# Optimization experiments

Hardware: AMD Instinct MI355X
Metric: run time of the kernel (lower is better)

The kernel has to match this reference:

```python
import jax, jax.numpy as jnp
import numpy as np

D = 512; N = 4096; NH = 16; DEPTH = 3; MLP = 4; GENES = 250; GH = 64; GW = 64


def setup_inputs() -> dict:
    key = jax.random.key(0)
    ks = jax.random.split(key, 10)
    gf = jax.random.normal(ks[0], (N, D), jnp.float32)
    # unique spot positions: permutation of the 64x64 grid cells
    perm = jax.random.permutation(ks[1], GH * GW)[:N]
    coords = jnp.stack([perm // GW, perm % GW], axis=1).astype(jnp.int32)
    s = 0.02
    rn = lambda k, sh: jax.random.normal(k, sh, jnp.float32) * s
    return dict(
        global_feats=gf, coords=coords, grid_h=GH, grid_w=GW,
        ln1_g=jnp.ones((DEPTH, D)), ln1_b=jnp.zeros((DEPTH, D)),
        wqkv=rn(ks[2], (DEPTH, 3 * D, D)), bqkv=jnp.zeros((DEPTH, 3 * D)),
        wo=rn(ks[3], (DEPTH, D, D)), bo=jnp.zeros((DEPTH, D)),
        ln2_g=jnp.ones((DEPTH, D)), ln2_b=jnp.zeros((DEPTH, D)),
        w1=rn(ks[4], (DEPTH, MLP * D, D)), b1=jnp.zeros((DEPTH, MLP * D)),
        w2=rn(ks[5], (DEPTH, D, MLP * D)), b2=jnp.zeros((DEPTH, D)),
        ck=rn(ks[6], (DEPTH, D, 1, 3, 3)), cb=jnp.zeros((DEPTH, D)),
        lnf_g=jnp.ones((D,)), lnf_b=jnp.zeros((D,)),
        wp=rn(ks[7], (GENES, D)), bp=jnp.zeros((GENES,)),
    )


def _ln(x, g, b, eps=1e-5):
    m = jnp.mean(x, axis=-1, keepdims=True)
    v = jnp.var(x, axis=-1, keepdims=True)
    return (x - m) * jax.lax.rsqrt(v + eps) * g + b


def reference(global_feats, coords, grid_h, grid_w, ln1_g, ln1_b, wqkv, bqkv,
              wo, bo, ln2_g, ln2_b, w1, b1, w2, b2, ck, cb, lnf_g, lnf_b, wp, bp):
    x = global_feats  # [N, D]
    n, d = x.shape
    nh = NH; dh = d // nh
    rows = coords[:, 0]; cols = coords[:, 1]
    for i in range(ln1_g.shape[0]):
        # --- self-attention (eval mode, dropout off) ---
        xn = _ln(x, ln1_g[i], ln1_b[i])
        qkv = xn @ wqkv[i].T + bqkv[i]                      # [N, 3D]
        q, k, v = jnp.split(qkv, 3, axis=-1)
        q = q.reshape(n, nh, dh).transpose(1, 0, 2)        # [H, N, dh]
        k = k.reshape(n, nh, dh).transpose(1, 0, 2)
        v = v.reshape(n, nh, dh).transpose(1, 0, 2)
        att = jax.nn.softmax(jnp.einsum('hqd,hkd->hqk', q, k) * (dh ** -0.5), axis=-1)
        ao = jnp.einsum('hqk,hkd->hqd', att, v).transpose(1, 0, 2).reshape(n, d)
        x = x + (ao @ wo[i].T + bo[i])
        # --- MLP ---
        h = jax.nn.gelu(_ln(x, ln2_g[i], ln2_b[i]) @ w1[i].T + b1[i], approximate=False)
        x = x + (h @ w2[i].T + b2[i])
        # --- APEG: scatter -> depthwise conv -> gather ---
        grid = jnp.zeros((d, grid_h, grid_w), x.dtype).at[:, rows, cols].set(x.T)
        co = jax.lax.conv_general_dilated(
            grid[None], ck[i], window_strides=(1, 1), padding=((1, 1), (1, 1)),
            dimension_numbers=('NCHW', 'OIHW', 'NCHW'), feature_group_count=d)[0]
        co = co + cb[i][:, None, None]
        x = x + co[:, rows, cols].T
    x = _ln(x, lnf_g, lnf_b)
    pred = x @ wp.T + bp
    return (x, pred)
```

## Files before the change

### kernel.cpp

```cpp
#include <hip/hip_runtime.h>
#include <math.h>

#define D 512
#define N_TOK 4096
#define NHEAD 16
#define DH 32
#define DEPTH 3
#define MLPD 2048
#define GENES 250
#define GH 64
#define GW 64

typedef __attribute__((ext_vector_type(8))) short short8;
typedef __attribute__((ext_vector_type(4))) float f32x4;
typedef unsigned short ushort_t;

#define AS1 __attribute__((address_space(1)))
#define AS3 __attribute__((address_space(3)))

#if defined(__has_builtin)
#if __has_builtin(__builtin_amdgcn_exp2f)
#define EXP2F(x) __builtin_amdgcn_exp2f(x)
#endif
#endif
#ifndef EXP2F
#define EXP2F(x) __expf(0.69314718056f * (x))
#endif

__device__ __forceinline__ unsigned short f2bf(float f) {
  unsigned int u = __float_as_uint(f);
  u += 0x7fffu + ((u >> 16) & 1u);
  return (unsigned short)(u >> 16);
}
__device__ __forceinline__ unsigned int bfpack(float a, float b) {
  return __builtin_amdgcn_perm(__float_as_uint(b), __float_as_uint(a), 0x07060302u);
}
__device__ __forceinline__ void gload_lds16(const ushort_t* g, ushort_t* l) {
  __builtin_amdgcn_global_load_lds(
      (const AS1 unsigned int*)g,
      (AS3 unsigned int*)(unsigned int)(unsigned long long)l, 16, 0, 0);
}
__device__ __forceinline__ int perm64(int m) {
  int mi = m >> 4, g = (m >> 2) & 3, r = m & 3;
  return ((mi & 1) << 5) | (g << 3) | ((mi >> 1) << 2) | r;
}

__global__ __launch_bounds__(256) void ln_kernel(const float* __restrict__ x,
    const float* __restrict__ g, const float* __restrict__ b,
    float* __restrict__ yf, ushort_t* __restrict__ ybf) {
  int row = blockIdx.x;
  int t = threadIdx.x;
  const float* xr = x + (size_t)row * D;
  float v0 = xr[t], v1 = xr[t + 256];
  float s = v0 + v1;
  float sq = v0 * v0 + v1 * v1;
#pragma unroll
  for (int off = 32; off > 0; off >>= 1) {
    s += __shfl_down(s, off, 64);
    sq += __shfl_down(sq, off, 64);
  }
  __shared__ float s1[4], s2[4];
  int wid = t >> 6, lane = t & 63;
  if (lane == 0) { s1[wid] = s; s2[wid] = sq; }
  __syncthreads();
  float tot = s1[0] + s1[1] + s1[2] + s1[3];
  float totq = s2[0] + s2[1] + s2[2] + s2[3];
  float mean = tot * (1.0f / D);
  float var = totq * (1.0f / D) - mean * mean;
  float rs = rsqrtf(var + 1e-5f);
  float r0 = (v0 - mean) * rs * g[t] + b[t];
  float r1 = (v1 - mean) * rs * g[t + 256] + b[t + 256];
  if (yf) { yf[(size_t)row * D + t] = r0; yf[(size_t)row * D + t + 256] = r1; }
  if (ybf) {
    ybf[(size_t)row * D + t] = f2bf(r0);
    ybf[(size_t)row * D + t + 256] = f2bf(r1);
  }
}

template <int TM, int TN, int NKH>
__global__ __launch_bounds__(256) void gemm_bf(
    const ushort_t* __restrict__ A, const ushort_t* __restrict__ B,
    const float* __restrict__ bias, const float* __restrict__ res,
    float* __restrict__ C, ushort_t* __restrict__ Cbf,
    ushort_t* __restrict__ qO, ushort_t* __restrict__ kO, ushort_t* __restrict__ vO,
    int K, int ldc, int nstore, int mode) {
  constexpr int MI = TM / 32;
  constexpr int NI = TN / 32;
  __shared__ ushort_t As[2][NKH][TM * 32];
  __shared__ ushort_t Bs[2][NKH][TN * 32];
  int t = threadIdx.x;
  int w = t >> 6, lane = t & 63;
  int g = lane >> 4, c = lane & 15;
  int orig = blockIdx.y * gridDim.x + blockIdx.x;
  int cpx = (gridDim.x * gridDim.y) >> 3;
  int wid2 = (orig & 7) * cpx + (orig >> 3);
  int bn = (wid2 % gridDim.x) * TN;
  int bm = (wid2 / gridDim.x) * TM;
  int wr = (w >> 1) * (TM / 2);
  int wc = (w & 1) * (TN / 2);

  const ushort_t* gA = A + (size_t)(bm + (t >> 2)) * K + (t & 3) * 8;
  const ushort_t* gB = B + (size_t)(bn + (t >> 2)) * K + (t & 3) * 8;

  auto stage = [&](int p, int koff) {
#pragma unroll
    for (int h = 0; h < NKH; ++h) {
      gload_lds16(gA + koff + h * 32, &As[p][h][t * 8]);
      if (TM == 128)
        gload_lds16(gA + koff + h * 32 + (size_t)64 * K, &As[p][h][(t + 256) * 8]);
      gload_lds16(gB + koff + h * 32, &Bs[p][h][t * 8]);
      if (TN == 128)
        gload_lds16(gB + koff + h * 32 + (size_t)64 * K, &Bs[p][h][(t + 256) * 8]);
    }
  };

  f32x4 acc[MI][NI] = {};

  const int niter = K / (32 * NKH);
  stage(0, 0);
  __syncthreads();
  for (int it = 0; it < niter; ++it) {
    int p = it & 1;
    if (it + 1 < niter) stage(p ^ 1, (it + 1) * 32 * NKH);
#pragma unroll
    for (int kh = 0; kh < NKH; ++kh) {
      short8 af[MI], bfr[NI];
#pragma unroll
      for (int mi = 0; mi < MI; ++mi)
        af[mi] = *(const short8*)&As[p][kh][(wr + mi * 16 + c) * 32 + g * 8];
#pragma unroll
      for (int ni = 0; ni < NI; ++ni)
        bfr[ni] = *(const short8*)&Bs[p][kh][(wc + ni * 16 + c) * 32 + g * 8];
#pragma unroll
      for (int mi = 0; mi < MI; ++mi)
#pragma unroll
        for (int ni = 0; ni < NI; ++ni)
          acc[mi][ni] = __builtin_amdgcn_mfma_f32_16x16x32_bf16(
              af[mi], bfr[ni], acc[mi][ni], 0, 0, 0);
    }
    __syncthreads();
  }

  const float qs_scale = 0.17677669529663688f * 1.4426950408889634f;
  if (mode == 2) {
#pragma unroll
    for (int ni = 0; ni < NI; ++ni) {
      int col = bn + wc + ni * 16 + c;
      float bv = bias[col];
      int which = col >> 9;
      int h = (col >> 5) & 15;
      int d = col & 31;
      size_t hb = (size_t)h * (N_TOK * DH);
#pragma unroll
      for (int mi = 0; mi < MI; ++mi) {
        int row0 = bm + wr + mi * 16 + g * 4;
        float v0 = acc[mi][ni][0] + bv;
        float v1 = acc[mi][ni][1] + bv;
        float v2 = acc[mi][ni][2] + bv;
        float v3 = acc[mi][ni][3] + bv;
        if (which == 0) {
          qO[hb + (size_t)(row0 + 0) * DH + d] = f2bf(v0 * qs_scale);
          qO[hb + (size_t)(row0 + 1) * DH + d] = f2bf(v1 * qs_scale);
          qO[hb + (size_t)(row0 + 2) * DH + d] = f2bf(v2 * qs_scale);
          qO[hb + (size_t)(row0 + 3) * DH + d] = f2bf(v3 * qs_scale);
        } else if (which == 1) {
          kO[hb + (size_t)(row0 + 0) * DH + d] = f2bf(v0);
          kO[hb + (size_t)(row0 + 1) * DH + d] = f2bf(v1);
          kO[hb + (size_t)(row0 + 2) * DH + d] = f2bf(v2);
          kO[hb + (size_t)(row0 + 3) * DH + d] = f2bf(v3);
        } else {
          int m = row0 & 63;
          int mi_l = m >> 4, g_l = (m >> 2) & 3;
          int nb = ((mi_l & 1) << 5) | (g_l << 3) | ((mi_l >> 1) << 2);
          uint2 pk;
          pk.x = (unsigned)f2bf(v0) | ((unsigned)f2bf(v1) << 16);
          pk.y = (unsigned)f2bf(v2) | ((unsigned)f2bf(v3) << 16);
          *(uint2*)(vO + hb + (size_t)d * N_TOK + (row0 & ~63) + nb) = pk;
        }
      }
    }
    return;
  }
#pragma unroll
  for (int ni = 0; ni < NI; ++ni) {
    int col = bn + wc + ni * 16 + c;
    float bv = bias[col];
    bool cok = col < nstore;
#pragma unroll
    for (int mi = 0; mi < MI; ++mi) {
      int row0 = bm + wr + mi * 16 + g * 4;
#pragma unroll
      for (int reg = 0; reg < 4; ++reg) {
        int row = row0 + reg;
        float v = acc[mi][ni][reg] + bv;
        if (mode == 0) {
          size_t idx = (size_t)row * ldc + col;
          if (cok) {
            if (res) v += res[idx];
            C[idx] = v;
          }
        } else {
          v = 0.5f * v * (1.0f + erff(v * 0.70710678118654752f));
          Cbf[(size_t)row * ldc + col] = f2bf(v);
        }
      }
    }
  }
}

#define KST 40
#define VTST 72

__global__ __launch_bounds__(256) void attn_mfma(
    const ushort_t* __restrict__ qb, const ushort_t* __restrict__ kb,
    const ushort_t* __restrict__ vtb, ushort_t* __restrict__ ao) {
  __shared__ ushort_t Ks[64 * KST];
  __shared__ ushort_t Vts[32 * VTST];
  int qt = blockIdx.x, head = blockIdx.y;
  int t = threadIdx.x;
  int w = t >> 6, lane = t & 63;
  int g = lane >> 4, c = lane & 15;
  const size_t hbase = (size_t)head * (N_TOK * DH);
  int q0 = qt * 128 + w * 32;

  short8 qf[2];
  qf[0] = *(const short8*)(qb + hbase + (size_t)(q0 + c) * DH + g * 8);
  qf[1] = *(const short8*)(qb + hbase + (size_t)(q0 + 16 + c) * DH + g * 8);

  short8 ones;
#pragma unroll
  for (int i = 0; i < 8; ++i) ones[i] = (short)0x3F80;

  f32x4 o[2][2] = {};
  f32x4 lf[2] = {};
  const f32x4 zf = {0.f, 0.f, 0.f, 0.f};

  const ushort_t* kg = kb + hbase + (size_t)(t >> 2) * DH + (t & 3) * 8;
  const ushort_t* vg = vtb + hbase + (size_t)(t >> 3) * N_TOK + (t & 7) * 8;
  ushort_t* kw = &Ks[(t >> 2) * KST + (t & 3) * 8];
  ushort_t* vw = &Vts[(t >> 3) * VTST + (t & 7) * 8];

  short8 kreg = *(const short8*)kg;
  short8 vreg = *(const short8*)vg;

  typedef union { short8 s8; unsigned int u32[4]; } pk_t;

  for (int tile = 0; tile < N_TOK / 64; ++tile) {
    __syncthreads();
    *(short8*)kw = kreg;
    *(short8*)vw = vreg;
    __syncthreads();
    if (tile + 1 < N_TOK / 64) {
      kreg = *(const short8*)(kg + (size_t)(tile + 1) * 64 * DH);
      vreg = *(const short8*)(vg + (tile + 1) * 64);
    }

    short8 kf[4];
#pragma unroll
    for (int mi = 0; mi < 4; ++mi)
      kf[mi] = *(const short8*)&Ks[(mi * 16 + c) * KST + g * 8];
    short8 vf[2][2];
#pragma unroll
    for (int half = 0; half < 2; ++half)
#pragma unroll
      for (int ch = 0; ch < 2; ++ch)
        vf[half][ch] = *(const short8*)&Vts[(half * 16 + c) * VTST + ch * 32 + g * 8];

    short8 pf[2][2];
#pragma unroll
    for (int qs = 0; qs < 2; ++qs) {
      f32x4 sp[4];
#pragma unroll
      for (int mi = 0; mi < 4; ++mi)
        sp[mi] = __builtin_amdgcn_mfma_f32_16x16x32_bf16(kf[mi], qf[qs], zf, 0, 0, 0);
      float pr[4][4];
#pragma unroll
      for (int mi = 0; mi < 4; ++mi)
#pragma unroll
        for (int r = 0; r < 4; ++r) pr[mi][r] = EXP2F(sp[mi][r]);
      pk_t p0, p1;
      p0.u32[0] = bfpack(pr[0][0], pr[0][1]);
      p0.u32[1] = bfpack(pr[0][2], pr[0][3]);
      p0.u32[2] = bfpack(pr[2][0], pr[2][1]);
      p0.u32[3] = bfpack(pr[2][2], pr[2][3]);
      p1.u32[0] = bfpack(pr[1][0], pr[1][1]);
      p1.u32[1] = bfpack(pr[1][2], pr[1][3]);
      p1.u32[2] = bfpack(pr[3][0], pr[3][1]);
      p1.u32[3] = bfpack(pr[3][2], pr[3][3]);
      pf[qs][0] = p0.s8;
      pf[qs][1] = p1.s8;
    }

#pragma unroll
    for (int qs = 0; qs < 2; ++qs) {
#pragma unroll
      for (int ch = 0; ch < 2; ++ch) {
        lf[qs] = __builtin_amdgcn_mfma_f32_16x16x32_bf16(ones, pf[qs][ch], lf[qs], 0, 0, 0);
#pragma unroll
        for (int half = 0; half < 2; ++half)
          o[qs][half] = __builtin_amdgcn_mfma_f32_16x16x32_bf16(
              vf[half][ch], pf[qs][ch], o[qs][half], 0, 0, 0);
      }
    }
  }

#pragma unroll
  for (int qs = 0; qs < 2; ++qs) {
    float inv = 1.0f / lf[qs][0];
    int q = q0 + qs * 16 + c;
    ushort_t* op = ao + (size_t)q * D + head * DH;
#pragma unroll
    for (int half = 0; half < 2; ++half)
#pragma unroll
      for (int reg = 0; reg < 4; ++reg)
        op[half * 16 + g * 4 + reg] = f2bf(o[qs][half][reg] * inv);
  }
}

__global__ void scatter_kernel(const int* __restrict__ coords,
                               int* __restrict__ pos2tok) {
  int n = blockIdx.x * 256 + threadIdx.x;
  if (n < N_TOK) pos2tok[coords[2 * n] * GW + coords[2 * n + 1]] = n;
}

__global__ __launch_bounds__(256) void conv_ln_kernel(
    const float* __restrict__ xin, float* __restrict__ xout,
    const float* __restrict__ ck, const float* __restrict__ cb,
    const int* __restrict__ pos2tok, const int* __restrict__ coords,
    const float* __restrict__ g, const float* __restrict__ b,
    float* __restrict__ yf, ushort_t* __restrict__ ybf) {
  int n = blockIdx.x, t = threadIdx.x;
  __shared__ int nb[9];
  if (t < 9) {
    int r = coords[2 * n], c = coords[2 * n + 1];
    int dy = t / 3 - 1, dx = t % 3 - 1;
    int rr = r + dy, cc = c + dx;
    nb[t] = (rr >= 0 && rr < GH && cc >= 0 && cc < GW) ? pos2tok[rr * GW + cc] : -1;
  }
  __syncthreads();
  float v[2];
#pragma unroll
  for (int j = 0; j < 2; ++j) {
    int ch = t + j * 256;
    float s = cb[ch];
#pragma unroll
    for (int tap = 0; tap < 9; ++tap) {
      int tok = nb[tap];
      if (tok >= 0) s = fmaf(ck[ch * 9 + tap], xin[(size_t)tok * D + ch], s);
    }
    v[j] = xin[(size_t)n * D + ch] + s;
    xout[(size_t)n * D + ch] = v[j];
  }
  float s = v[0] + v[1];
  float sq = v[0] * v[0] + v[1] * v[1];
#pragma unroll
  for (int off = 32; off > 0; off >>= 1) {
    s += __shfl_down(s, off, 64);
    sq += __shfl_down(sq, off, 64);
  }
  __shared__ float s1[4], s2[4];
  int wid = t >> 6, lane = t & 63;
  if (lane == 0) { s1[wid] = s; s2[wid] = sq; }
  __syncthreads();
  float tot = s1[0] + s1[1] + s1[2] + s1[3];
  float totq = s2[0] + s2[1] + s2[2] + s2[3];
  float mean = tot * (1.0f / D);
  float var = totq * (1.0f / D) - mean * mean;
  float rs = rsqrtf(var + 1e-5f);
  float r0 = (v[0] - mean) * rs * g[t] + b[t];
  float r1 = (v[1] - mean) * rs * g[t + 256] + b[t + 256];
  if (yf) { yf[(size_t)n * D + t] = r0; yf[(size_t)n * D + t + 256] = r1; }
  ybf[(size_t)n * D + t] = f2bf(r0);
  ybf[(size_t)n * D + t + 256] = f2bf(r1);
}

__global__ __launch_bounds__(256) void castw(const float* __restrict__ src,
    ushort_t* __restrict__ dst, int n_src, int n_dst) {
  int i = (blockIdx.x * 256 + threadIdx.x) * 4;
  if (i >= n_dst) return;
  unsigned long long pk = 0;
#pragma unroll
  for (int j = 0; j < 4; ++j) {
    float v = (i + j < n_src) ? src[i + j] : 0.f;
    pk |= ((unsigned long long)f2bf(v)) << (16 * j);
  }
  *(unsigned long long*)(dst + i) = pk;
}

__global__ void pad_bias(const float* __restrict__ src, float* __restrict__ dst) {
  int i = threadIdx.x;
  dst[i] = (i < GENES) ? src[i] : 0.f;
}

extern "C" void kernel_launch(void* const* d_in, const int* in_sizes, int n_in,
                              void* d_out, int out_size, void* d_ws, size_t ws_size,
                              hipStream_t stream) {
  const float* gf     = (const float*)d_in[0];
  const int*   coords = (const int*)d_in[1];
  const float* ln1_g  = (const float*)d_in[4];
  const float* ln1_b  = (const float*)d_in[5];
  const float* wqkv   = (const float*)d_in[6];
  const float* bqkv   = (const float*)d_in[7];
  const float* wo     = (const float*)d_in[8];
  const float* bo     = (const float*)d_in[9];
  const float* ln2_g  = (const float*)d_in[10];
  const float* ln2_b  = (const float*)d_in[11];
  const float* w1     = (const float*)d_in[12];
  const float* b1     = (const float*)d_in[13];
  const float* w2     = (const float*)d_in[14];
  const float* b2     = (const float*)d_in[15];
  const float* ck     = (const float*)d_in[16];
  const float* cb     = (const float*)d_in[17];
  const float* lnf_g  = (const float*)d_in[18];
  const float* lnf_b  = (const float*)d_in[19];
  const float* wp     = (const float*)d_in[20];
  const float* bp     = (const float*)d_in[21];
  float* out = (float*)d_out;

  const size_t ND = (size_t)N_TOK * D;
  float* xb0 = (float*)d_ws;
  float* xb1 = xb0 + ND;
  ushort_t* xn_bf  = (ushort_t*)(xb1 + ND);
  ushort_t* ao_bf  = xn_bf + ND;
  ushort_t* out_bf = ao_bf + ND;
  ushort_t* shared = out_bf + ND;
  ushort_t* qb   = shared;
  ushort_t* kbuf = qb + ND;
  ushort_t* vtb  = kbuf + ND;
  ushort_t* h_bf = shared;
  ushort_t* wqkv_bf = shared + (size_t)N_TOK * MLPD;
  ushort_t* wo_bf = wqkv_bf + DEPTH * 3 * D * D;
  ushort_t* w1_bf = wo_bf + DEPTH * D * D;
  ushort_t* w2_bf = w1_bf + DEPTH * MLPD * D;
  ushort_t* wp_bf = w2_bf + DEPTH * D * MLPD;
  float* bp_pad = (float*)(wp_bf + 256 * D);
  int* pos2tok = (int*)(bp_pad + 256);

  hipMemcpyAsync(xb0, gf, ND * sizeof(float), hipMemcpyDeviceToDevice, stream);
  hipMemsetAsync(pos2tok, 0xFF, GH * GW * sizeof(int), stream);
  scatter_kernel<<<(N_TOK + 255) / 256, 256, 0, stream>>>(coords, pos2tok);

  int nw;
  nw = DEPTH * 3 * D * D;  castw<<<(nw / 4 + 255) / 256, 256, 0, stream>>>(wqkv, wqkv_bf, nw, nw);
  nw = DEPTH * D * D;      castw<<<(nw / 4 + 255) / 256, 256, 0, stream>>>(wo, wo_bf, nw, nw);
  nw = DEPTH * MLPD * D;   castw<<<(nw / 4 + 255) / 256, 256, 0, stream>>>(w1, w1_bf, nw, nw);
  nw = DEPTH * D * MLPD;   castw<<<(nw / 4 + 255) / 256, 256, 0, stream>>>(w2, w2_bf, nw, nw);
  castw<<<(256 * D / 4 + 255) / 256, 256, 0, stream>>>(wp, wp_bf, GENES * D, 256 * D);
  pad_bias<<<1, 256, 0, stream>>>(bp, bp_pad);

  ln_kernel<<<N_TOK, 256, 0, stream>>>(xb0, ln1_g, ln1_b, nullptr, xn_bf);

  float* x  = xb0;
  float* xo = xb1;
  for (int i = 0; i < DEPTH; ++i) {
    gemm_bf<128, 64, 2><<<dim3(24, 32), 256, 0, stream>>>(
        xn_bf, wqkv_bf + (size_t)i * 3 * D * D, bqkv + (size_t)i * 3 * D,
        nullptr, nullptr, nullptr, qb, kbuf, vtb, D, 0, 3 * D, 2);
    attn_mfma<<<dim3(N_TOK / 128, NHEAD), 256, 0, stream>>>(qb, kbuf, vtb, ao_bf);
    gemm_bf<64, 64, 2><<<dim3(8, 64), 256, 0, stream>>>(
        ao_bf, wo_bf + (size_t)i * D * D, bo + (size_t)i * D,
        x, x, nullptr, nullptr, nullptr, nullptr, D, D, D, 0);
    ln_kernel<<<N_TOK, 256, 0, stream>>>(x, ln2_g + i * D, ln2_b + i * D, nullptr, xn_bf);
    gemm_bf<128, 128, 2><<<dim3(16, 32), 256, 0, stream>>>(
        xn_bf, w1_bf + (size_t)i * MLPD * D, b1 + (size_t)i * MLPD,
        nullptr, nullptr, h_bf, nullptr, nullptr, nullptr, D, MLPD, MLPD, 1);
    gemm_bf<64, 64, 4><<<dim3(8, 64), 256, 0, stream>>>(
        h_bf, w2_bf + (size_t)i * D * MLPD, b2 + (size_t)i * D,
        x, x, nullptr, nullptr, nullptr, nullptr, MLPD, D, D, 0);
    if (i < DEPTH - 1) {
      conv_ln_kernel<<<N_TOK, 256, 0, stream>>>(
          x, xo, ck + (size_t)i * D * 9, cb + (size_t)i * D, pos2tok, coords,
          ln1_g + (i + 1) * D, ln1_b + (i + 1) * D, nullptr, xn_bf);
    } else {
      conv_ln_kernel<<<N_TOK, 256, 0, stream>>>(
          x, xo, ck + (size_t)i * D * 9, cb + (size_t)i * D, pos2tok, coords,
          lnf_g, lnf_b, out, out_bf);
    }
    float* tmp = x; x = xo; xo = tmp;
  }
  gemm_bf<64, 64, 2><<<dim3(4, 64), 256, 0, stream>>>(
      out_bf, wp_bf, bp_pad, nullptr, out + ND, nullptr, nullptr, nullptr, nullptr,
      D, GENES, GENES, 0);
}
```

Baseline: 592.5 us.

## Split-K the output-projection and MLP-down GEMMs with atomic accumulation into residual

```diff
diff --git a/kernel.cpp b/kernel.cpp
--- a/kernel.cpp
+++ b/kernel.cpp
@@ -99,18 +99,21 @@
   int wr = (w >> 1) * (TM / 2);
   int wc = (w & 1) * (TN / 2);
 
-  const ushort_t* gA = A + (size_t)(bm + (t >> 2)) * K + (t & 3) * 8;
-  const ushort_t* gB = B + (size_t)(bn + (t >> 2)) * K + (t & 3) * 8;
+  const size_t Kld = (size_t)K * gridDim.z;
+  const int koff0 = blockIdx.z * K;
+
+  const ushort_t* gA = A + (size_t)(bm + (t >> 2)) * Kld + koff0 + (t & 3) * 8;
+  const ushort_t* gB = B + (size_t)(bn + (t >> 2)) * Kld + koff0 + (t & 3) * 8;
 
   auto stage = [&](int p, int koff) {
 #pragma unroll
     for (int h = 0; h < NKH; ++h) {
       gload_lds16(gA + koff + h * 32, &As[p][h][t * 8]);
       if (TM == 128)
-        gload_lds16(gA + koff + h * 32 + (size_t)64 * K, &As[p][h][(t + 256) * 8]);
+        gload_lds16(gA + koff + h * 32 + (size_t)64 * Kld, &As[p][h][(t + 256) * 8]);
       gload_lds16(gB + koff + h * 32, &Bs[p][h][t * 8]);
       if (TN == 128)
-        gload_lds16(gB + koff + h * 32 + (size_t)64 * K, &Bs[p][h][(t + 256) * 8]);
+        gload_lds16(gB + koff + h * 32 + (size_t)64 * Kld, &Bs[p][h][(t + 256) * 8]);
     }
   };
 
@@ -181,6 +184,24 @@
     }
     return;
   }
+  if (mode == 3) {
+    bool addb = (blockIdx.z == 0);
+#pragma unroll
+    for (int ni = 0; ni < NI; ++ni) {
+      int col = bn + wc + ni * 16 + c;
+      float bv = addb ? bias[col] : 0.f;
+#pragma unroll
+      for (int mi = 0; mi < MI; ++mi) {
+        int row0 = bm + wr + mi * 16 + g * 4;
+#pragma unroll
+        for (int reg = 0; reg < 4; ++reg) {
+          size_t idx = (size_t)(row0 + reg) * ldc + col;
+          atomicAdd(&C[idx], acc[mi][ni][reg] + bv);
+        }
+      }
+    }
+    return;
+  }
 #pragma unroll
   for (int ni = 0; ni < NI; ++ni) {
     int col = bn + wc + ni * 16 + c;
@@ -457,16 +478,16 @@
         xn_bf, wqkv_bf + (size_t)i * 3 * D * D, bqkv + (size_t)i * 3 * D,
         nullptr, nullptr, nullptr, qb, kbuf, vtb, D, 0, 3 * D, 2);
     attn_mfma<<<dim3(N_TOK / 128, NHEAD), 256, 0, stream>>>(qb, kbuf, vtb, ao_bf);
-    gemm_bf<64, 64, 2><<<dim3(8, 64), 256, 0, stream>>>(
+    gemm_bf<64, 64, 2><<<dim3(8, 64, 2), 256, 0, stream>>>(
         ao_bf, wo_bf + (size_t)i * D * D, bo + (size_t)i * D,
-        x, x, nullptr, nullptr, nullptr, nullptr, D, D, D, 0);
+        nullptr, x, nullptr, nullptr, nullptr, nullptr, D / 2, D, D, 3);
     ln_kernel<<<N_TOK, 256, 0, stream>>>(x, ln2_g + i * D, ln2_b + i * D, nullptr, xn_bf);
     gemm_bf<128, 128, 2><<<dim3(16, 32), 256, 0, stream>>>(
         xn_bf, w1_bf + (size_t)i * MLPD * D, b1 + (size_t)i * MLPD,
         nullptr, nullptr, h_bf, nullptr, nullptr, nullptr, D, MLPD, MLPD, 1);
-    gemm_bf<64, 64, 4><<<dim3(8, 64), 256, 0, stream>>>(
+    gemm_bf<64, 64, 2><<<dim3(8, 64, 2), 256, 0, stream>>>(
         h_bf, w2_bf + (size_t)i * D * MLPD, b2 + (size_t)i * D,
-        x, x, nullptr, nullptr, nullptr, nullptr, MLPD, D, D, 0);
+        nullptr, x, nullptr, nullptr, nullptr, nullptr, MLPD / 2, D, D, 3);
     if (i < DEPTH - 1) {
       conv_ln_kernel<<<N_TOK, 256, 0, stream>>>(
           x, xo, ck + (size_t)i * D * 9, cb + (size_t)i * D, pos2tok, coords,
```

After: 625.4 us. 5.6% more time.
